# Kernel optimization log

Hardware: AMD Instinct MI355X
Metric: run time of the kernel (lower is better)

The kernel has to match this reference:

```python
import jax, jax.numpy as jnp
import numpy as np

N_COMPRESS = 2048
N_EXPAND_QK = 1024
N_EXPAND_V = 1024
TOPK_C, TOPK_QK, TOPK_V = 8, 4, 6


def _topk_sparsify(w, k):
    # top-k along last dim, scatter back, renormalize (matches torch scatter_ path)
    vals, idx = jax.lax.top_k(w, k)                      # [B,k]
    rows = jnp.arange(w.shape[0])[:, None]
    sparse = jnp.zeros_like(w).at[rows, idx].set(vals)   # [B,N]
    return sparse / (sparse.sum(axis=-1, keepdims=True) + 1e-8)


def setup_inputs() -> dict:
    key = jax.random.key(0)
    k0, k1, k2, k3 = jax.random.split(key, 4)
    B, S, D, DS = 4, 4096, 2048, 64
    total = N_COMPRESS + N_EXPAND_QK + N_EXPAND_V
    return {
        "x": jax.random.normal(k0, (B, S, D), jnp.float32),
        "importance": jax.random.uniform(k1, (B, S), jnp.float32),
        "W": jax.random.normal(k2, (D, DS), jnp.float32) * 0.02,
        "b": jnp.zeros((DS,), jnp.float32),
        "neuron_emb": jax.random.normal(k3, (total, DS), jnp.float32) * 0.02,
    }


def reference(x, importance, W, b, neuron_emb):
    # projection (dropout is identity in eval mode)
    h = x @ W + b                                             # [B,S,ds]
    # cosine logits against unit-norm neuron embeddings
    emb_n = neuron_emb / jnp.linalg.norm(neuron_emb, axis=-1, keepdims=True)
    all_logits = jnp.einsum('bsd,nd->bsn', h, emb_n)          # [B,S,total]
    lC = all_logits[..., :N_COMPRESS]
    lQK = all_logits[..., N_COMPRESS:N_COMPRESS + N_EXPAND_QK]
    lV = all_logits[..., N_COMPRESS + N_EXPAND_QK:]
    pC = jax.nn.softmax(lC, axis=-1)
    pQK = jax.nn.softmax(lQK, axis=-1)   # expand_Q and expand_K share the slice (eval: identical)
    pV = jax.nn.softmax(lV, axis=-1)
    # importance-weighted pooling to per-batch dense routing weights
    dC = jnp.einsum('bs,bsn->bn', importance, pC)
    dQK = jnp.einsum('bs,bsn->bn', importance, pQK)
    dV = jnp.einsum('bs,bsn->bn', importance, pV)
    wC = _topk_sparsify(dC, TOPK_C)
    wQ = _topk_sparsify(dQK, TOPK_QK)
    wK = _topk_sparsify(dQK, TOPK_QK)
    wV = _topk_sparsify(dV, TOPK_V)
    # concat the four routing-weight outputs: [B, 2048+1024+1024+1024]
    return jnp.concatenate([wC, wQ, wK, wV], axis=-1)
```

## Files before the change

### kernel.cpp

```cpp
#include <hip/hip_runtime.h>
#include <math.h>

#define D_IN   2048

typedef __bf16 bf16x8 __attribute__((ext_vector_type(8)));
typedef float  f32x4  __attribute__((ext_vector_type(4)));

__global__ __launch_bounds__(256) void k_prep(const float* __restrict__ emb,
                                              const float* __restrict__ W,
                                              __bf16* __restrict__ e_hi,
                                              __bf16* __restrict__ e_lo,
                                              __bf16* __restrict__ wt_hi,
                                              __bf16* __restrict__ wt_lo) {
    int blk = blockIdx.x, t = threadIdx.x;
    if (blk < 1024) {
        int gid  = blk * 256 + t;
        int row  = gid >> 6;
        int lane = gid & 63;
        float v  = emb[row * 64 + lane];
        float ss = v * v;
#pragma unroll
        for (int m = 32; m >= 1; m >>= 1) ss += __shfl_xor(ss, m);
        float nv = v / sqrtf(ss);
        __bf16 hb = (__bf16)nv;
        e_hi[row * 64 + lane] = hb;
        e_lo[row * 64 + lane] = (__bf16)(nv - (float)hb);
    } else {
        int gid = (blk - 1024) * 256 + t;
        int c   = gid >> 11;
        int k   = gid & 2047;
        float v = W[k * 64 + c];
        __bf16 hb = (__bf16)v;
        wt_hi[c * 2048 + k] = hb;
        wt_lo[c * 2048 + k] = (__bf16)(v - (float)hb);
    }
}

#define CHUNK_MFMA(N0)                                                        \
    {                                                                         \
        bf16x8 bh[2][2];                                                      \
        _Pragma("unroll") for (int ct = 0; ct < 2; ++ct)                      \
        _Pragma("unroll") for (int ks = 0; ks < 2; ++ks)                      \
            bh[ct][ks] = *(const bf16x8*)(e_hi +                              \
                (size_t)((N0) + ct * 16 + l15) * 64 + ks * 32 + kg * 8);      \
        _Pragma("unroll") for (int rt = 0; rt < 2; ++rt)                      \
        _Pragma("unroll") for (int ct = 0; ct < 2; ++ct)                      \
        _Pragma("unroll") for (int ks = 0; ks < 2; ++ks)                      \
            acc[rt][ct] = __builtin_amdgcn_mfma_f32_16x16x32_bf16(            \
                a_hi[rt][ks], bh[ct][ks], acc[rt][ct], 0, 0, 0);              \
        _Pragma("unroll") for (int rt = 0; rt < 2; ++rt)                      \
        _Pragma("unroll") for (int ct = 0; ct < 2; ++ct)                      \
        _Pragma("unroll") for (int ks = 0; ks < 2; ++ks)                      \
            acc[rt][ct] = __builtin_amdgcn_mfma_f32_16x16x32_bf16(            \
                a_lo[rt][ks], bh[ct][ks], acc[rt][ct], 0, 0, 0);              \
        bf16x8 bl[2][2];                                                      \
        _Pragma("unroll") for (int ct = 0; ct < 2; ++ct)                      \
        _Pragma("unroll") for (int ks = 0; ks < 2; ++ks)                      \
            bl[ct][ks] = *(const bf16x8*)(e_lo +                              \
                (size_t)((N0) + ct * 16 + l15) * 64 + ks * 32 + kg * 8);      \
        _Pragma("unroll") for (int rt = 0; rt < 2; ++rt)                      \
        _Pragma("unroll") for (int ct = 0; ct < 2; ++ct)                      \
        _Pragma("unroll") for (int ks = 0; ks < 2; ++ks)                      \
            acc[rt][ct] = __builtin_amdgcn_mfma_f32_16x16x32_bf16(            \
                a_hi[rt][ks], bl[ct][ks], acc[rt][ct], 0, 0, 0);              \
    }

__global__ __launch_bounds__(512, 4) void k_fused(
        const float* __restrict__ x,
        const __bf16* __restrict__ wt_hi, const __bf16* __restrict__ wt_lo,
        const float* __restrict__ bias,
        const __bf16* __restrict__ e_hi, const __bf16* __restrict__ e_lo,
        const float* __restrict__ imp, float* __restrict__ partials) {
    __shared__ float  h_acc[32][66];
    __shared__ __bf16 hb_hi[32][64];
    __shared__ __bf16 hb_lo[32][64];
    __shared__ float  zs[8][4][8];

    int t    = threadIdx.x;
    int wave = t >> 6;
    int lane = t & 63;
    int l15  = lane & 15;
    int kg   = lane >> 4;
    int row0 = blockIdx.x * 32;

    for (int i = t; i < 32 * 66; i += 512) ((float*)h_acc)[i] = 0.f;
    __syncthreads();

    {
        f32x4 hacc[2][4] = {};
        int kb0 = wave * 256;
#pragma unroll 2
        for (int ks = 0; ks < 8; ++ks) {
            int kb = kb0 + ks * 32 + kg * 8;
            bf16x8 ah[2], al[2];
#pragma unroll
            for (int rt = 0; rt < 2; ++rt) {
                const float* xp = x + (size_t)(row0 + rt * 16 + l15) * D_IN + kb;
                float4 a0 = *(const float4*)xp;
                float4 a1 = *(const float4*)(xp + 4);
                float av[8] = {a0.x, a0.y, a0.z, a0.w, a1.x, a1.y, a1.z, a1.w};
#pragma unroll
                for (int j = 0; j < 8; ++j) {
                    __bf16 hb = (__bf16)av[j];
                    ah[rt][j] = hb;
                    al[rt][j] = (__bf16)(av[j] - (float)hb);
                }
            }
            bf16x8 bh[4];
#pragma unroll
            for (int ct = 0; ct < 4; ++ct)
                bh[ct] = *(const bf16x8*)(wt_hi + (size_t)(ct * 16 + l15) * D_IN + kb);
#pragma unroll
            for (int rt = 0; rt < 2; ++rt)
#pragma unroll
                for (int ct = 0; ct < 4; ++ct)
                    hacc[rt][ct] = __builtin_amdgcn_mfma_f32_16x16x32_bf16(
                        ah[rt], bh[ct], hacc[rt][ct], 0, 0, 0);
#pragma unroll
            for (int rt = 0; rt < 2; ++rt)
#pragma unroll
                for (int ct = 0; ct < 4; ++ct)
                    hacc[rt][ct] = __builtin_amdgcn_mfma_f32_16x16x32_bf16(
                        al[rt], bh[ct], hacc[rt][ct], 0, 0, 0);
            bf16x8 bl[4];
#pragma unroll
            for (int ct = 0; ct < 4; ++ct)
                bl[ct] = *(const bf16x8*)(wt_lo + (size_t)(ct * 16 + l15) * D_IN + kb);
#pragma unroll
            for (int rt = 0; rt < 2; ++rt)
#pragma unroll
                for (int ct = 0; ct < 4; ++ct)
                    hacc[rt][ct] = __builtin_amdgcn_mfma_f32_16x16x32_bf16(
                        ah[rt], bl[ct], hacc[rt][ct], 0, 0, 0);
        }
#pragma unroll
        for (int rt = 0; rt < 2; ++rt)
#pragma unroll
            for (int ct = 0; ct < 4; ++ct)
#pragma unroll
                for (int r = 0; r < 4; ++r)
                    atomicAdd(&h_acc[rt * 16 + kg * 4 + r][ct * 16 + l15],
                              hacc[rt][ct][r]);
    }
    __syncthreads();
    if (wave == 0) {
#pragma unroll 4
        for (int row = 0; row < 32; ++row) {
            float v = h_acc[row][lane] + bias[lane];
            __bf16 hb = (__bf16)v;
            int c2 = ((((lane >> 3) ^ (row & 7)) << 3) | (lane & 7));
            hb_hi[row][c2] = hb;
            hb_lo[row][c2] = (__bf16)(v - (float)hb);
        }
    }
    __syncthreads();

    bf16x8 a_hi[2][2], a_lo[2][2];
#pragma unroll
    for (int rt = 0; rt < 2; ++rt)
#pragma unroll
        for (int ks = 0; ks < 2; ++ks) {
            int row = rt * 16 + l15;
            int g   = ((ks * 4 + kg) ^ (l15 & 7)) * 8;
            a_hi[rt][ks] = *(const bf16x8*)&hb_hi[row][g];
            a_lo[rt][ks] = *(const bf16x8*)&hb_lo[row][g];
        }

    int b    = blockIdx.x >> 7;
    int slot = blockIdx.x & 127;
    float* pbase = partials + ((size_t)(b * 128 + slot)) * 4096;

    const int segB[4] = {0, 2048, 3072, 4096};
    for (int sg = 0; sg < 3; ++sg) {
        float zc[2][4] = {};
        for (int nb = segB[sg]; nb < segB[sg + 1]; nb += 256) {
            int n0 = nb + wave * 32;
            f32x4 acc[2][2] = {};
            CHUNK_MFMA(n0)
#pragma unroll
            for (int rt = 0; rt < 2; ++rt)
#pragma unroll
                for (int r = 0; r < 4; ++r)
                    zc[rt][r] += __expf(acc[rt][0][r]) + __expf(acc[rt][1][r]);
        }
#pragma unroll
        for (int rt = 0; rt < 2; ++rt)
#pragma unroll
            for (int r = 0; r < 4; ++r) {
                float z = zc[rt][r];
#pragma unroll
                for (int m = 1; m < 16; m <<= 1) z += __shfl_xor(z, m);
                zc[rt][r] = z;
            }
        if (l15 == 0) {
#pragma unroll
            for (int rt = 0; rt < 2; ++rt)
#pragma unroll
                for (int r = 0; r < 4; ++r)
                    zs[wave][kg][rt * 4 + r] = zc[rt][r];
        }
        __syncthreads();
        float cf[2][4];
#pragma unroll
        for (int rt = 0; rt < 2; ++rt)
#pragma unroll
            for (int r = 0; r < 4; ++r) {
                float z = 0.f;
#pragma unroll
                for (int w = 0; w < 8; ++w) z += zs[w][kg][rt * 4 + r];
                cf[rt][r] = imp[row0 + rt * 16 + kg * 4 + r] / z;
            }
        __syncthreads();
        for (int nb = segB[sg]; nb < segB[sg + 1]; nb += 256) {
            int n0 = nb + wave * 32;
            f32x4 acc[2][2] = {};
            CHUNK_MFMA(n0)
            float s0 = 0.f, s1 = 0.f;
#pragma unroll
            for (int rt = 0; rt < 2; ++rt)
#pragma unroll
                for (int r = 0; r < 4; ++r) {
                    s0 += cf[rt][r] * __expf(acc[rt][0][r]);
                    s1 += cf[rt][r] * __expf(acc[rt][1][r]);
                }
            s0 += __shfl_xor(s0, 16); s0 += __shfl_xor(s0, 32);
            s1 += __shfl_xor(s1, 16); s1 += __shfl_xor(s1, 32);
            if (kg == 0) {
                pbase[n0 + l15]      = s0;
                pbase[n0 + 16 + l15] = s1;
            }
        }
    }
}

__global__ __launch_bounds__(256) void k_topk(const float* __restrict__ partials,
                                              float* __restrict__ out) {
    __shared__ float dv[2048];
    __shared__ float redv[4];
    __shared__ int   redi[4];
    __shared__ float selv[8];
    __shared__ int   seli[8];
    int blk = blockIdx.x;
    int b   = blk / 3;
    int sg  = blk - 3 * b;
    int t   = threadIdx.x;
    const int segStart[3] = {0, 2048, 3072};
    const int segLen[3]   = {2048, 1024, 1024};
    const int segK[3]     = {8, 4, 6};
    const int segOut[3]   = {0, 2048, 4096};
    int st = segStart[sg], len = segLen[sg], kk = segK[sg];
    for (int n = t; n < len; n += 256) {
        const float* p = partials + (size_t)b * 128 * 4096 + st + n;
        float s0 = 0.f, s1 = 0.f, s2 = 0.f, s3 = 0.f;
#pragma unroll 4
        for (int sl = 0; sl < 128; sl += 4) {
            s0 += p[(size_t)(sl + 0) * 4096];
            s1 += p[(size_t)(sl + 1) * 4096];
            s2 += p[(size_t)(sl + 2) * 4096];
            s3 += p[(size_t)(sl + 3) * 4096];
        }
        dv[n] = (s0 + s1) + (s2 + s3);
    }
    __syncthreads();
    for (int it = 0; it < kk; ++it) {
        float bv = -3.0e38f;
        int   bi = 1 << 30;
        for (int n = t; n < len; n += 256) {
            float v = dv[n];
            if (v > bv) { bv = v; bi = n; }
        }
#pragma unroll
        for (int m = 1; m < 64; m <<= 1) {
            float ov = __shfl_xor(bv, m);
            int   oi = __shfl_xor(bi, m);
            if (ov > bv || (ov == bv && oi < bi)) { bv = ov; bi = oi; }
        }
        if ((t & 63) == 0) { redv[t >> 6] = bv; redi[t >> 6] = bi; }
        __syncthreads();
        if (t == 0) {
            for (int w = 1; w < 4; ++w)
                if (redv[w] > bv || (redv[w] == bv && redi[w] < bi)) {
                    bv = redv[w]; bi = redi[w];
                }
            selv[it] = bv;
            seli[it] = bi;
            dv[bi] = -3.4e38f;
        }
        __syncthreads();
    }
    float sum = 0.f;
    for (int it = 0; it < kk; ++it) sum += selv[it];
    float inv = 1.0f / (sum + 1e-8f);
    for (int n = t; n < len; n += 256) {
        float v = 0.0f;
        for (int it = 0; it < kk; ++it)
            if (seli[it] == n) v = selv[it] * inv;
        out[b * 5120 + segOut[sg] + n] = v;
        if (sg == 1) out[b * 5120 + 3072 + n] = v;
    }
}

extern "C" void kernel_launch(void* const* d_in, const int* in_sizes, int n_in,
                              void* d_out, int out_size, void* d_ws, size_t ws_size,
                              hipStream_t stream) {
    (void)in_sizes; (void)n_in; (void)out_size; (void)ws_size;
    const float* x    = (const float*)d_in[0];
    const float* imp  = (const float*)d_in[1];
    const float* W    = (const float*)d_in[2];
    const float* bias = (const float*)d_in[3];
    const float* emb  = (const float*)d_in[4];
    float* out = (float*)d_out;

    char* w = (char*)d_ws;
    __bf16* e_hi  = (__bf16*)w;  w += (size_t)4096 * 64 * 2;
    __bf16* e_lo  = (__bf16*)w;  w += (size_t)4096 * 64 * 2;
    __bf16* wt_hi = (__bf16*)w;  w += (size_t)64 * 2048 * 2;
    __bf16* wt_lo = (__bf16*)w;  w += (size_t)64 * 2048 * 2;
    float*  partials = (float*)w; w += (size_t)4 * 128 * 4096 * 4;

    hipLaunchKernelGGL(k_prep,  dim3(1536), dim3(256), 0, stream,
                       emb, W, e_hi, e_lo, wt_hi, wt_lo);
    hipLaunchKernelGGL(k_fused, dim3(512),  dim3(512), 0, stream,
                       x, wt_hi, wt_lo, bias, e_hi, e_lo, imp, partials);
    hipLaunchKernelGGL(k_topk,  dim3(12),   dim3(256), 0, stream,
                       partials, out);
}
```

Before: 450.9 us.

## Software-pipeline x and embedding loads, replace partials buffer with global atomics

The projection loop is fully unrolled with double-buffered x loads so that the next k-slice's global loads are issued before the current slice's MFMAs. The logit passes now prefetch the next embedding chunk's hi/lo fragments while the current chunk's MFMAs run. The per-block partial sums buffer (4x128x4096 floats) is replaced by atomicAdd into a 4x4096 accumulator that k_prep zeroes. This removes the 128-way reduction from the single-wave-per-segment topk kernel, at the cost of atomic contention and nondeterministic summation order.

```diff
diff --git a/kernel.cpp b/kernel.cpp
--- a/kernel.cpp
+++ b/kernel.cpp
@@ -5,13 +5,16 @@
 
 typedef __bf16 bf16x8 __attribute__((ext_vector_type(8)));
 typedef float  f32x4  __attribute__((ext_vector_type(4)));
+
+#define mfma16 __builtin_amdgcn_mfma_f32_16x16x32_bf16
 
 __global__ __launch_bounds__(256) void k_prep(const float* __restrict__ emb,
                                               const float* __restrict__ W,
                                               __bf16* __restrict__ e_hi,
                                               __bf16* __restrict__ e_lo,
                                               __bf16* __restrict__ wt_hi,
-                                              __bf16* __restrict__ wt_lo) {
+                                              __bf16* __restrict__ wt_lo,
+                                              float* __restrict__ dacc) {
     int blk = blockIdx.x, t = threadIdx.x;
     if (blk < 1024) {
         int gid  = blk * 256 + t;
@@ -25,7 +28,7 @@
         __bf16 hb = (__bf16)nv;
         e_hi[row * 64 + lane] = hb;
         e_lo[row * 64 + lane] = (__bf16)(nv - (float)hb);
-    } else {
+    } else if (blk < 1536) {
         int gid = (blk - 1024) * 256 + t;
         int c   = gid >> 11;
         int k   = gid & 2047;
@@ -33,44 +36,17 @@
         __bf16 hb = (__bf16)v;
         wt_hi[c * 2048 + k] = hb;
         wt_lo[c * 2048 + k] = (__bf16)(v - (float)hb);
+    } else {
+        dacc[(blk - 1536) * 256 + t] = 0.f;
     }
 }
-
-#define CHUNK_MFMA(N0)                                                        \
-    {                                                                         \
-        bf16x8 bh[2][2];                                                      \
-        _Pragma("unroll") for (int ct = 0; ct < 2; ++ct)                      \
-        _Pragma("unroll") for (int ks = 0; ks < 2; ++ks)                      \
-            bh[ct][ks] = *(const bf16x8*)(e_hi +                              \
-                (size_t)((N0) + ct * 16 + l15) * 64 + ks * 32 + kg * 8);      \
-        _Pragma("unroll") for (int rt = 0; rt < 2; ++rt)                      \
-        _Pragma("unroll") for (int ct = 0; ct < 2; ++ct)                      \
-        _Pragma("unroll") for (int ks = 0; ks < 2; ++ks)                      \
-            acc[rt][ct] = __builtin_amdgcn_mfma_f32_16x16x32_bf16(            \
-                a_hi[rt][ks], bh[ct][ks], acc[rt][ct], 0, 0, 0);              \
-        _Pragma("unroll") for (int rt = 0; rt < 2; ++rt)                      \
-        _Pragma("unroll") for (int ct = 0; ct < 2; ++ct)                      \
-        _Pragma("unroll") for (int ks = 0; ks < 2; ++ks)                      \
-            acc[rt][ct] = __builtin_amdgcn_mfma_f32_16x16x32_bf16(            \
-                a_lo[rt][ks], bh[ct][ks], acc[rt][ct], 0, 0, 0);              \
-        bf16x8 bl[2][2];                                                      \
-        _Pragma("unroll") for (int ct = 0; ct < 2; ++ct)                      \
-        _Pragma("unroll") for (int ks = 0; ks < 2; ++ks)                      \
-            bl[ct][ks] = *(const bf16x8*)(e_lo +                              \
-                (size_t)((N0) + ct * 16 + l15) * 64 + ks * 32 + kg * 8);      \
-        _Pragma("unroll") for (int rt = 0; rt < 2; ++rt)                      \
-        _Pragma("unroll") for (int ct = 0; ct < 2; ++ct)                      \
-        _Pragma("unroll") for (int ks = 0; ks < 2; ++ks)                      \
-            acc[rt][ct] = __builtin_amdgcn_mfma_f32_16x16x32_bf16(            \
-                a_hi[rt][ks], bl[ct][ks], acc[rt][ct], 0, 0, 0);              \
-    }
 
 __global__ __launch_bounds__(512, 4) void k_fused(
         const float* __restrict__ x,
         const __bf16* __restrict__ wt_hi, const __bf16* __restrict__ wt_lo,
         const float* __restrict__ bias,
         const __bf16* __restrict__ e_hi, const __bf16* __restrict__ e_lo,
-        const float* __restrict__ imp, float* __restrict__ partials) {
+        const float* __restrict__ imp, float* __restrict__ dacc) {
     __shared__ float  h_acc[32][66];
     __shared__ __bf16 hb_hi[32][64];
     __shared__ __bf16 hb_lo[32][64];
@@ -82,57 +58,62 @@
     int l15  = lane & 15;
     int kg   = lane >> 4;
     int row0 = blockIdx.x * 32;
+    const f32x4 z4 = {0.f, 0.f, 0.f, 0.f};
 
     for (int i = t; i < 32 * 66; i += 512) ((float*)h_acc)[i] = 0.f;
     __syncthreads();
 
     {
-        f32x4 hacc[2][4] = {};
+        f32x4 hacc[2][4];
+#pragma unroll
+        for (int rt = 0; rt < 2; ++rt)
+#pragma unroll
+            for (int ct = 0; ct < 4; ++ct) hacc[rt][ct] = z4;
         int kb0 = wave * 256;
-#pragma unroll 2
-        for (int ks = 0; ks < 8; ++ks) {
-            int kb = kb0 + ks * 32 + kg * 8;
-            bf16x8 ah[2], al[2];
-#pragma unroll
-            for (int rt = 0; rt < 2; ++rt) {
-                const float* xp = x + (size_t)(row0 + rt * 16 + l15) * D_IN + kb;
-                float4 a0 = *(const float4*)xp;
-                float4 a1 = *(const float4*)(xp + 4);
-                float av[8] = {a0.x, a0.y, a0.z, a0.w, a1.x, a1.y, a1.z, a1.w};
-#pragma unroll
-                for (int j = 0; j < 8; ++j) {
-                    __bf16 hb = (__bf16)av[j];
-                    ah[rt][j] = hb;
-                    al[rt][j] = (__bf16)(av[j] - (float)hb);
-                }
-            }
-            bf16x8 bh[4];
-#pragma unroll
-            for (int ct = 0; ct < 4; ++ct)
-                bh[ct] = *(const bf16x8*)(wt_hi + (size_t)(ct * 16 + l15) * D_IN + kb);
-#pragma unroll
-            for (int rt = 0; rt < 2; ++rt)
-#pragma unroll
-                for (int ct = 0; ct < 4; ++ct)
-                    hacc[rt][ct] = __builtin_amdgcn_mfma_f32_16x16x32_bf16(
-                        ah[rt], bh[ct], hacc[rt][ct], 0, 0, 0);
-#pragma unroll
-            for (int rt = 0; rt < 2; ++rt)
-#pragma unroll
-                for (int ct = 0; ct < 4; ++ct)
-                    hacc[rt][ct] = __builtin_amdgcn_mfma_f32_16x16x32_bf16(
-                        al[rt], bh[ct], hacc[rt][ct], 0, 0, 0);
-            bf16x8 bl[4];
-#pragma unroll
-            for (int ct = 0; ct < 4; ++ct)
-                bl[ct] = *(const bf16x8*)(wt_lo + (size_t)(ct * 16 + l15) * D_IN + kb);
-#pragma unroll
-            for (int rt = 0; rt < 2; ++rt)
-#pragma unroll
-                for (int ct = 0; ct < 4; ++ct)
-                    hacc[rt][ct] = __builtin_amdgcn_mfma_f32_16x16x32_bf16(
-                        ah[rt], bl[ct], hacc[rt][ct], 0, 0, 0);
-        }
+        const float* xr0 = x + (size_t)(row0 + l15) * D_IN + kb0 + kg * 8;
+        const float* xr1 = xr0 + 16 * D_IN;
+        float4 xe0, xe1, xe2, xe3, xo0, xo1, xo2, xo3;
+
+#define LDX(B, KS) { B##0 = *(const float4*)(xr0 + (KS) * 32); \
+                     B##1 = *(const float4*)(xr0 + (KS) * 32 + 4); \
+                     B##2 = *(const float4*)(xr1 + (KS) * 32); \
+                     B##3 = *(const float4*)(xr1 + (KS) * 32 + 4); }
+#define CVT8(DH, DL, V0, V1) { \
+    float av[8] = {V0.x, V0.y, V0.z, V0.w, V1.x, V1.y, V1.z, V1.w}; \
+    _Pragma("unroll") for (int j = 0; j < 8; ++j) { \
+        __bf16 hb = (__bf16)av[j]; DH[j] = hb; \
+        DL[j] = (__bf16)(av[j] - (float)hb); } }
+#define HCOMP(B, KS) { \
+    bf16x8 ah[2], al[2], bw[4]; \
+    CVT8(ah[0], al[0], B##0, B##1) \
+    CVT8(ah[1], al[1], B##2, B##3) \
+    int kb = kb0 + (KS) * 32 + kg * 8; \
+    _Pragma("unroll") for (int ct = 0; ct < 4; ++ct) \
+        bw[ct] = *(const bf16x8*)(wt_hi + (size_t)(ct * 16 + l15) * D_IN + kb); \
+    _Pragma("unroll") for (int rt = 0; rt < 2; ++rt) \
+    _Pragma("unroll") for (int ct = 0; ct < 4; ++ct) \
+        hacc[rt][ct] = mfma16(ah[rt], bw[ct], hacc[rt][ct], 0, 0, 0); \
+    _Pragma("unroll") for (int rt = 0; rt < 2; ++rt) \
+    _Pragma("unroll") for (int ct = 0; ct < 4; ++ct) \
+        hacc[rt][ct] = mfma16(al[rt], bw[ct], hacc[rt][ct], 0, 0, 0); \
+    _Pragma("unroll") for (int ct = 0; ct < 4; ++ct) \
+        bw[ct] = *(const bf16x8*)(wt_lo + (size_t)(ct * 16 + l15) * D_IN + kb); \
+    _Pragma("unroll") for (int rt = 0; rt < 2; ++rt) \
+    _Pragma("unroll") for (int ct = 0; ct < 4; ++ct) \
+        hacc[rt][ct] = mfma16(ah[rt], bw[ct], hacc[rt][ct], 0, 0, 0); }
+
+        LDX(xe, 0)
+        LDX(xo, 1) HCOMP(xe, 0)
+        LDX(xe, 2) HCOMP(xo, 1)
+        LDX(xo, 3) HCOMP(xe, 2)
+        LDX(xe, 4) HCOMP(xo, 3)
+        LDX(xo, 5) HCOMP(xe, 4)
+        LDX(xe, 6) HCOMP(xo, 5)
+        LDX(xo, 7) HCOMP(xe, 6)
+        HCOMP(xo, 7)
+#undef LDX
+#undef HCOMP
+
 #pragma unroll
         for (int rt = 0; rt < 2; ++rt)
 #pragma unroll
@@ -166,22 +147,50 @@
             a_lo[rt][ks] = *(const bf16x8*)&hb_lo[row][g];
         }
 
-    int b    = blockIdx.x >> 7;
-    int slot = blockIdx.x & 127;
-    float* pbase = partials + ((size_t)(b * 128 + slot)) * 4096;
+    int bb = blockIdx.x >> 7;
+    float* dbase = dacc + bb * 4096;
+    const __bf16* pe_hi = e_hi + l15 * 64 + kg * 8;
+    const __bf16* pe_lo = e_lo + l15 * 64 + kg * 8;
+
+#define LOADH(P, NN) { size_t off = (size_t)(NN) * 64; \
+    P##H0 = *(const bf16x8*)(pe_hi + off); \
+    P##H1 = *(const bf16x8*)(pe_hi + off + 32); \
+    P##L0 = *(const bf16x8*)(pe_lo + off); \
+    P##L1 = *(const bf16x8*)(pe_lo + off + 32); }
+#define MFMAH(P, CT) { \
+    _Pragma("unroll") for (int rt = 0; rt < 2; ++rt) { \
+        f32x4 tt = acc[rt][CT]; \
+        tt = mfma16(a_hi[rt][0], P##H0, tt, 0, 0, 0); \
+        tt = mfma16(a_hi[rt][1], P##H1, tt, 0, 0, 0); \
+        tt = mfma16(a_lo[rt][0], P##H0, tt, 0, 0, 0); \
+        tt = mfma16(a_lo[rt][1], P##H1, tt, 0, 0, 0); \
+        tt = mfma16(a_hi[rt][0], P##L0, tt, 0, 0, 0); \
+        tt = mfma16(a_hi[rt][1], P##L1, tt, 0, 0, 0); \
+        acc[rt][CT] = tt; } }
+
+    bf16x8 qaH0, qaH1, qaL0, qaL1, qbH0, qbH1, qbL0, qbL1;
 
     const int segB[4] = {0, 2048, 3072, 4096};
     for (int sg = 0; sg < 3; ++sg) {
+        int sBeg = segB[sg];
+        int nc   = (segB[sg + 1] - sBeg) >> 8;
         float zc[2][4] = {};
-        for (int nb = segB[sg]; nb < segB[sg + 1]; nb += 256) {
-            int n0 = nb + wave * 32;
-            f32x4 acc[2][2] = {};
-            CHUNK_MFMA(n0)
-#pragma unroll
-            for (int rt = 0; rt < 2; ++rt)
-#pragma unroll
-                for (int r = 0; r < 4; ++r)
-                    zc[rt][r] += __expf(acc[rt][0][r]) + __expf(acc[rt][1][r]);
+        {
+            LOADH(qa, sBeg + wave * 32)
+            for (int c = 0; c < nc; ++c) {
+                int n0 = sBeg + c * 256 + wave * 32;
+                f32x4 acc[2][2];
+                acc[0][0] = z4; acc[0][1] = z4; acc[1][0] = z4; acc[1][1] = z4;
+                LOADH(qb, n0 + 16)
+                MFMAH(qa, 0)
+                if (c + 1 < nc) { LOADH(qa, n0 + 256) }
+                MFMAH(qb, 1)
+#pragma unroll
+                for (int rt = 0; rt < 2; ++rt)
+#pragma unroll
+                    for (int r = 0; r < 4; ++r)
+                        zc[rt][r] += __expf(acc[rt][0][r]) + __expf(acc[rt][1][r]);
+            }
         }
 #pragma unroll
         for (int rt = 0; rt < 2; ++rt)
@@ -211,29 +220,38 @@
                 cf[rt][r] = imp[row0 + rt * 16 + kg * 4 + r] / z;
             }
         __syncthreads();
-        for (int nb = segB[sg]; nb < segB[sg + 1]; nb += 256) {
-            int n0 = nb + wave * 32;
-            f32x4 acc[2][2] = {};
-            CHUNK_MFMA(n0)
-            float s0 = 0.f, s1 = 0.f;
-#pragma unroll
-            for (int rt = 0; rt < 2; ++rt)
-#pragma unroll
-                for (int r = 0; r < 4; ++r) {
-                    s0 += cf[rt][r] * __expf(acc[rt][0][r]);
-                    s1 += cf[rt][r] * __expf(acc[rt][1][r]);
+        {
+            LOADH(qa, sBeg + wave * 32)
+            for (int c = 0; c < nc; ++c) {
+                int n0 = sBeg + c * 256 + wave * 32;
+                f32x4 acc[2][2];
+                acc[0][0] = z4; acc[0][1] = z4; acc[1][0] = z4; acc[1][1] = z4;
+                LOADH(qb, n0 + 16)
+                MFMAH(qa, 0)
+                if (c + 1 < nc) { LOADH(qa, n0 + 256) }
+                MFMAH(qb, 1)
+                float s0 = 0.f, s1 = 0.f;
+#pragma unroll
+                for (int rt = 0; rt < 2; ++rt)
+#pragma unroll
+                    for (int r = 0; r < 4; ++r) {
+                        s0 += cf[rt][r] * __expf(acc[rt][0][r]);
+                        s1 += cf[rt][r] * __expf(acc[rt][1][r]);
+                    }
+                s0 += __shfl_xor(s0, 16); s0 += __shfl_xor(s0, 32);
+                s1 += __shfl_xor(s1, 16); s1 += __shfl_xor(s1, 32);
+                if (kg == 0) {
+                    atomicAdd(&dbase[n0 + l15],      s0);
+                    atomicAdd(&dbase[n0 + 16 + l15], s1);
                 }
-            s0 += __shfl_xor(s0, 16); s0 += __shfl_xor(s0, 32);
-            s1 += __shfl_xor(s1, 16); s1 += __shfl_xor(s1, 32);
-            if (kg == 0) {
-                pbase[n0 + l15]      = s0;
-                pbase[n0 + 16 + l15] = s1;
             }
         }
     }
+#undef LOADH
+#undef MFMAH
 }
 
-__global__ __launch_bounds__(256) void k_topk(const float* __restrict__ partials,
+__global__ __launch_bounds__(256) void k_topk(const float* __restrict__ dacc,
                                               float* __restrict__ out) {
     __shared__ float dv[2048];
     __shared__ float redv[4];
@@ -249,18 +267,7 @@
     const int segK[3]     = {8, 4, 6};
     const int segOut[3]   = {0, 2048, 4096};
     int st = segStart[sg], len = segLen[sg], kk = segK[sg];
-    for (int n = t; n < len; n += 256) {
-        const float* p = partials + (size_t)b * 128 * 4096 + st + n;
-        float s0 = 0.f, s1 = 0.f, s2 = 0.f, s3 = 0.f;
-#pragma unroll 4
-        for (int sl = 0; sl < 128; sl += 4) {
-            s0 += p[(size_t)(sl + 0) * 4096];
-            s1 += p[(size_t)(sl + 1) * 4096];
-            s2 += p[(size_t)(sl + 2) * 4096];
-            s3 += p[(size_t)(sl + 3) * 4096];
-        }
-        dv[n] = (s0 + s1) + (s2 + s3);
-    }
+    for (int n = t; n < len; n += 256) dv[n] = dacc[b * 4096 + st + n];
     __syncthreads();
     for (int it = 0; it < kk; ++it) {
         float bv = -3.0e38f;
@@ -316,12 +323,12 @@
     __bf16* e_lo  = (__bf16*)w;  w += (size_t)4096 * 64 * 2;
     __bf16* wt_hi = (__bf16*)w;  w += (size_t)64 * 2048 * 2;
     __bf16* wt_lo = (__bf16*)w;  w += (size_t)64 * 2048 * 2;
-    float*  partials = (float*)w; w += (size_t)4 * 128 * 4096 * 4;
-
-    hipLaunchKernelGGL(k_prep,  dim3(1536), dim3(256), 0, stream,
-                       emb, W, e_hi, e_lo, wt_hi, wt_lo);
+    float*  dacc  = (float*)w;   w += (size_t)4 * 4096 * 4;
+
+    hipLaunchKernelGGL(k_prep,  dim3(1600), dim3(256), 0, stream,
+                       emb, W, e_hi, e_lo, wt_hi, wt_lo, dacc);
     hipLaunchKernelGGL(k_fused, dim3(512),  dim3(512), 0, stream,
-                       x, wt_hi, wt_lo, bias, e_hi, e_lo, imp, partials);
+                       x, wt_hi, wt_lo, bias, e_hi, e_lo, imp, dacc);
     hipLaunchKernelGGL(k_topk,  dim3(12),   dim3(256), 0, stream,
-                       partials, out);
+                       dacc, out);
 }
```

New measurement: 363.2 us. 1.24x faster.
